# Kernel tuning notes

Hardware: AMD Instinct MI355X
Metric: run time of the kernel (lower is better)

Reference implementation:

```python
import jax, jax.numpy as jnp
import numpy as np

P = 2; NH = 8; NW = 4; NB = 6; D = 512; HID = 2048; NREG = 1; T = 1000; NACT = 3
HH = 32; WW = 32; C = 3; B = 1; DUR = 6


def _kron_bool(a, b):
    # kron(A,B)[i*p+k, j*q+l] = A[i,j] & B[k,l]
    m, n = a.shape; p, q = b.shape
    return (a[:, None, :, None] & b[None, :, None, :]).reshape(m * p, n * q)


def _masks(dur_zr, seq_zr, dur_xa, seq_xa):
    m_left = _kron_bool(jnp.eye(dur_zr, dtype=bool), jnp.ones((seq_zr, seq_zr), dtype=bool))
    tmp = jnp.ones((dur_zr, dur_zr), dtype=bool)
    band = jnp.tril(tmp, -1) ^ jnp.tril(tmp, -1 - NW)  # sliding window over previous frames
    m_right = _kron_bool(band[:, :-1], jnp.ones((seq_zr, seq_xa), dtype=bool))
    m_self = _kron_bool(jnp.tril(jnp.ones((dur_xa, dur_xa), dtype=bool)), jnp.ones((seq_xa, seq_xa), dtype=bool))
    return ~jnp.concatenate([m_left, m_right], axis=1), ~m_self


def _ln(x):
    mu = jnp.mean(x, -1, keepdims=True)
    xc = x - mu
    var = jnp.mean(xc * xc, -1, keepdims=True)
    return xc * jax.lax.rsqrt(var + 1e-5)


def _patch(x, Wp, bp):
    b, dur, c, h, w = x.shape
    x = x.reshape(b, dur, c, h // P, P, w // P, P)
    x = x.transpose(0, 1, 3, 5, 2, 4, 6).reshape(b, dur, (h // P) * (w // P), c * P * P)
    return x @ Wp + bp


def _unpatch(x, Wu, bu):
    b, dur, s, d = x.shape
    y = x @ Wu + bu  # [b,dur,s,C*P*P]
    y = y.reshape(b, dur, HH // P, WW // P, C, P, P)
    return y.transpose(0, 1, 4, 2, 5, 3, 6).reshape(b, dur, C, HH, WW)


def _mod(x, cond, Wm, bm):
    # AdaLN: per-frame scale/shift broadcast over tokens of that frame
    scale, shift = jnp.split(jax.nn.silu(cond) @ Wm + bm, 2, axis=-1)
    b, L, d = x.shape; dur = cond.shape[1]; s = L // dur
    y = _ln(x).reshape(b, dur, s, d)
    return (y * (1.0 + scale[:, :, None]) + shift[:, :, None]).reshape(b, L, d)


def _gate(x, cond, Wg, bg):
    g = cond @ Wg + bg
    b, L, d = x.shape; dur = cond.shape[1]; s = L // dur
    return (x.reshape(b, dur, s, d) * g[:, :, None]).reshape(b, L, d)


def _attn(q, kv, mask, Wq, bq, Wk, bk, Wv, bv, Wo, bo):
    b, lq, d = q.shape; lk = kv.shape[1]; dh = d // NH
    qh = (q @ Wq + bq).reshape(b, lq, NH, dh)
    kh = (kv @ Wk + bk).reshape(b, lk, NH, dh)
    vh = (kv @ Wv + bv).reshape(b, lk, NH, dh)
    s = jnp.einsum('bqhd,bkhd->bhqk', qh, kh) * (1.0 / np.sqrt(dh))
    s = jnp.where(mask[None, None], -1e9, s)  # mask True = disallowed
    o = jnp.einsum('bhqk,bkhd->bqhd', jax.nn.softmax(s, axis=-1), vh)
    return o.reshape(b, lq, d) @ Wo + bo


def _geglu(x, Wg, bg, Wo, bo):
    a, g = jnp.split(x @ Wg + bg, 2, axis=-1)
    return (a * jax.nn.gelu(g, approximate=False)) @ Wo + bo


def _forward(z, frames, actions, ts, W_patch, b_patch, W_unpatch, b_unpatch, registers, pe_grid, action_emb, time_emb, W_mod1, b_mod1, W_mod2, b_mod2, W_q, b_q, W_k, b_k, W_v, b_v, W_o, b_o, W_g1, b_g1, W_g2, b_g2, W_geglu, b_geglu, W_ffout, b_ffout):
    zt = _patch(z, W_patch, b_patch) + pe_grid[None, None]
    xt = _patch(frames, W_patch, b_patch) + pe_grid[None, None]
    a = action_emb[actions]  # [B, dur, D]
    b, dur_zr, s, d = zt.shape
    zr = jnp.concatenate([zt, jnp.broadcast_to(registers[None, None], (b, dur_zr, NREG, d))], axis=2)
    xa = jnp.concatenate([xt, a[:, :-1, None, :]], axis=2)
    seq_zr = zr.shape[2]; dur_xa = xa.shape[1]; seq_xa = xa.shape[2]
    mask_cross, mask_self = _masks(dur_zr, seq_zr, dur_xa, seq_xa)
    zr = zr.reshape(b, dur_zr * seq_zr, d)
    xa = xa.reshape(b, dur_xa * seq_xa, d)
    cond = time_emb[ts]  # [B, dur_zr, D]
    clean = jnp.broadcast_to(time_emb[0][None, None], (b, dur_xa, d))
    for i in range(NB):
        zrn = _mod(zr, cond, W_mod1[i], b_mod1[i])
        xan = _mod(xa, clean, W_mod1[i], b_mod1[i])
        xkv = jnp.concatenate([zrn, xan], axis=1)
        cross = _attn(zrn, xkv, mask_cross, W_q[i], b_q[i], W_k[i], b_k[i], W_v[i], b_v[i], W_o[i], b_o[i])
        selfa = _attn(xan, xan, mask_self, W_q[i], b_q[i], W_k[i], b_k[i], W_v[i], b_v[i], W_o[i], b_o[i])
        zr = _gate(zrn, cond, W_g1[i], b_g1[i])
        xa = _gate(xan, clean, W_g1[i], b_g1[i])
        zr = _mod(zr + cross, cond, W_mod2[i], b_mod2[i])
        xa = _mod(xa + selfa, clean, W_mod2[i], b_mod2[i])
        zr = _geglu(zr, W_geglu[i], b_geglu[i], W_ffout[i], b_ffout[i])
        xa = _geglu(xa, W_geglu[i], b_geglu[i], W_ffout[i], b_ffout[i])
        zr = _gate(zr, cond, W_g2[i], b_g2[i])
        xa = _gate(xa, clean, W_g2[i], b_g2[i])
    zr = zr.reshape(b, dur_zr, seq_zr, d)[:, :, :-NREG]
    return _unpatch(zr, W_unpatch, b_unpatch)


def setup_inputs() -> dict:
    key = jax.random.key(0)
    ks = iter(jax.random.split(key, 64))
    def rn(shape, scale=0.02):
        return jax.random.normal(next(ks), shape, dtype=jnp.float32) * scale
    inp = {}
    inp['z'] = jax.random.normal(next(ks), (B, DUR, C, HH, WW), dtype=jnp.float32)
    inp['frames'] = jax.random.normal(next(ks), (B, DUR - 1, C, HH, WW), dtype=jnp.float32)
    inp['actions'] = jax.random.randint(next(ks), (B, DUR), 0, NACT)
    inp['ts'] = jax.random.randint(next(ks), (B, DUR), 0, T)
    inp['W_patch'] = rn((C * P * P, D)); inp['b_patch'] = jnp.zeros((D,), jnp.float32)
    inp['W_unpatch'] = rn((D, C * P * P)); inp['b_unpatch'] = jnp.zeros((C * P * P,), jnp.float32)
    inp['registers'] = rn((NREG, D), 1.0 / D ** 0.5)
    inp['pe_grid'] = rn(((HH // P) * (WW // P), D), 1.0 / D ** 0.5)
    inp['action_emb'] = rn((NACT, D), 1.0)
    inp['time_emb'] = rn((T, D), 1.0)
    inp['W_mod1'] = rn((NB, D, 2 * D)); inp['b_mod1'] = jnp.zeros((NB, 2 * D), jnp.float32)
    inp['W_mod2'] = rn((NB, D, 2 * D)); inp['b_mod2'] = jnp.zeros((NB, 2 * D), jnp.float32)
    for nm in ('q', 'k', 'v', 'o'):
        inp['W_' + nm] = rn((NB, D, D)); inp['b_' + nm] = jnp.zeros((NB, D), jnp.float32)
    inp['W_g1'] = rn((NB, D, D)); inp['b_g1'] = jnp.ones((NB, D), jnp.float32)
    inp['W_g2'] = rn((NB, D, D)); inp['b_g2'] = jnp.ones((NB, D), jnp.float32)
    inp['W_geglu'] = rn((NB, D, 2 * HID)); inp['b_geglu'] = jnp.zeros((NB, 2 * HID), jnp.float32)
    inp['W_ffout'] = rn((NB, HID, D)); inp['b_ffout'] = jnp.zeros((NB, D), jnp.float32)
    return inp


def reference(z, frames, actions, ts, W_patch, b_patch, W_unpatch, b_unpatch, registers, pe_grid, action_emb, time_emb, W_mod1, b_mod1, W_mod2, b_mod2, W_q, b_q, W_k, b_k, W_v, b_v, W_o, b_o, W_g1, b_g1, W_g2, b_g2, W_geglu, b_geglu, W_ffout, b_ffout):
    return _forward(z, frames, actions, ts, W_patch, b_patch, W_unpatch, b_unpatch, registers, pe_grid, action_emb, time_emb, W_mod1, b_mod1, W_mod2, b_mod2, W_q, b_q, W_k, b_k, W_v, b_v, W_o, b_o, W_g1, b_g1, W_g2, b_g2, W_geglu, b_geglu, W_ffout, b_ffout)
```

## Files before the change

### kernel.cpp

```cpp
#include <hip/hip_runtime.h>
#include <hip/hip_bf16.h>
#include <math.h>

#define DURZ 6
#define DURX 5
#define SEQ 257
#define LZ 1542
#define LX 1285
#define LT 2827
#define DM 512
#define NHEADS 8
#define DH 64
#define HIDDEN 2048

typedef __bf16 bf16x8 __attribute__((ext_vector_type(8)));
typedef __bf16 bf16x4 __attribute__((ext_vector_type(4)));
typedef float f32x4 __attribute__((ext_vector_type(4)));

__global__ void fill_kernel(float* __restrict__ out, int n, float v) {
    int i = blockIdx.x * blockDim.x + threadIdx.x;
    if (i < n) out[i] = v;
}

__global__ void embed_kernel(const float* __restrict__ z,
                             const float* __restrict__ frames,
                             const int* __restrict__ actions,
                             const float* __restrict__ W_patch,
                             const float* __restrict__ b_patch,
                             const float* __restrict__ registers,
                             const float* __restrict__ pe,
                             const float* __restrict__ action_emb,
                             float* __restrict__ state) {
    int T = blockIdx.x;
    int tid = threadIdx.x;
    bool is_z = T < LZ;
    int T2 = is_z ? T : T - LZ;
    int f = T2 / SEQ, t = T2 % SEQ;
    if (t < 256) {
        const float* src = is_z ? z : frames;
        int hp = t >> 4, wp = t & 15;
        float pv[12];
#pragma unroll
        for (int c = 0; c < 3; c++)
#pragma unroll
            for (int ph = 0; ph < 2; ph++)
#pragma unroll
                for (int pw = 0; pw < 2; pw++)
                    pv[c * 4 + ph * 2 + pw] =
                        src[((f * 3 + c) * 32 + (hp * 2 + ph)) * 32 + (wp * 2 + pw)];
        for (int d = tid; d < DM; d += 256) {
            float acc = b_patch[d];
#pragma unroll
            for (int j = 0; j < 12; j++) acc += pv[j] * W_patch[j * DM + d];
            acc += pe[t * DM + d];
            state[T * DM + d] = acc;
        }
    } else if (is_z) {
        for (int d = tid; d < DM; d += 256) state[T * DM + d] = registers[d];
    } else {
        int a = actions[f];
        for (int d = tid; d < DM; d += 256) state[T * DM + d] = action_emb[a * DM + d];
    }
}

__global__ void cond_kernel(const int* __restrict__ ts,
                            const float* __restrict__ time_emb,
                            float* __restrict__ condraw,
                            float* __restrict__ condsilu) {
    int idx = blockIdx.x * blockDim.x + threadIdx.x;
    if (idx >= 7 * 512) return;
    int r = idx >> 9;
    int j = idx & 511;
    int tsr = (r < 6) ? ts[r] : 0;
    float x = time_emb[tsr * 512 + j];
    condraw[idx] = x;
    condsilu[idx] = x / (1.0f + expf(-x));
}

__global__ void params_kernel(const float* __restrict__ condraw,
                              const float* __restrict__ condsilu,
                              const float* __restrict__ W_mod1,
                              const float* __restrict__ b_mod1,
                              const float* __restrict__ W_mod2,
                              const float* __restrict__ b_mod2,
                              const float* __restrict__ W_g1,
                              const float* __restrict__ b_g1,
                              const float* __restrict__ W_g2,
                              const float* __restrict__ b_g2,
                              float* __restrict__ params) {
    int idx = blockIdx.x * blockDim.x + threadIdx.x;
    if (idx >= 6 * 7 * 3072) return;
    int i = idx / 21504;
    int rem = idx % 21504;
    int r = rem / 3072;
    int c = rem % 3072;
    const float* cv;
    const float* W;
    float bias;
    int ldw;
    if (c < 1024) {
        cv = condsilu + r * 512;
        W = W_mod1 + (size_t)i * 512 * 1024 + c; ldw = 1024;
        bias = b_mod1[i * 1024 + c];
    } else if (c < 2048) {
        int cc = c - 1024;
        cv = condsilu + r * 512;
        W = W_mod2 + (size_t)i * 512 * 1024 + cc; ldw = 1024;
        bias = b_mod2[i * 1024 + cc];
    } else if (c < 2560) {
        int cc = c - 2048;
        cv = condraw + r * 512;
        W = W_g1 + (size_t)i * 512 * 512 + cc; ldw = 512;
        bias = b_g1[i * 512 + cc];
    } else {
        int cc = c - 2560;
        cv = condraw + r * 512;
        W = W_g2 + (size_t)i * 512 * 512 + cc; ldw = 512;
        bias = b_g2[i * 512 + cc];
    }
    float acc = bias;
    for (int j = 0; j < 512; j++) acc += cv[j] * W[(size_t)j * ldw];
    params[idx] = acc;
}

template<bool PL>
__global__ __launch_bounds__(256) void lnmod_kernel(const float* __restrict__ xf,
                                                    const __bf16* __restrict__ xh,
                                                    const __bf16* __restrict__ xl,
                                                    __bf16* __restrict__ yh,
                                                    __bf16* __restrict__ yl,
                                                    const float* __restrict__ params,
                                                    int mod_off) {
    int T = blockIdx.x;
    int tid = threadIdx.x;
    int r = (T < LZ) ? (T / SEQ) : 6;
    const float* prow = params + r * 3072 + mod_off;
    size_t base = (size_t)T * DM;
    float v0, v1;
    if constexpr (PL) {
        v0 = (float)xh[base + tid] + (float)xl[base + tid];
        v1 = (float)xh[base + tid + 256] + (float)xl[base + tid + 256];
    } else {
        v0 = xf[base + tid];
        v1 = xf[base + tid + 256];
    }
    float s_ = v0 + v1, q_ = v0 * v0 + v1 * v1;
#pragma unroll
    for (int off = 32; off; off >>= 1) {
        s_ += __shfl_down(s_, off);
        q_ += __shfl_down(q_, off);
    }
    __shared__ float sh[8];
    int wave = tid >> 6, lane = tid & 63;
    if (lane == 0) { sh[wave] = s_; sh[4 + wave] = q_; }
    __syncthreads();
    float sum = sh[0] + sh[1] + sh[2] + sh[3];
    float sq = sh[4] + sh[5] + sh[6] + sh[7];
    float mu = sum * (1.0f / 512.0f);
    float var = sq * (1.0f / 512.0f) - mu * mu;
    float rstd = rsqrtf(var + 1e-5f);
    float y0 = (v0 - mu) * rstd * (1.0f + prow[tid]) + prow[512 + tid];
    float y1 = (v1 - mu) * rstd * (1.0f + prow[tid + 256]) + prow[512 + tid + 256];
    __bf16 h0 = (__bf16)y0, h1 = (__bf16)y1;
    yh[base + tid] = h0;
    yl[base + tid] = (__bf16)(y0 - (float)h0);
    yh[base + tid + 256] = h1;
    yl[base + tid + 256] = (__bf16)(y1 - (float)h1);
}


#define MFMA3(accv, ah, al, bh, bl)                                            \
    accv = __builtin_amdgcn_mfma_f32_16x16x32_bf16(al, bh, accv, 0, 0, 0);     \
    accv = __builtin_amdgcn_mfma_f32_16x16x32_bf16(ah, bl, accv, 0, 0, 0);     \
    accv = __builtin_amdgcn_mfma_f32_16x16x32_bf16(ah, bh, accv, 0, 0, 0);

__global__ __launch_bounds__(256) void wprep_kernel(const float* __restrict__ Wq,
                                                    const float* __restrict__ Wk,
                                                    const float* __restrict__ Wv,
                                                    const float* __restrict__ Wo,
                                                    const float* __restrict__ Wglu,
                                                    const float* __restrict__ Wff,
                                                    float* __restrict__ Wp) {
    __shared__ __align__(16) __bf16 T[2][64][40];
    int id = blockIdx.x, t = threadIdx.x;
    const float* src;
    int N, nsub, kt;
    size_t dstf;
    if (id < 512) {
        int mat = id >> 7, rem = id & 127;
        nsub = rem >> 4; kt = rem & 15; N = 512;
        src = mat == 0 ? Wq : mat == 1 ? Wk : mat == 2 ? Wv : Wo;
        dstf = (size_t)mat * 327680 + (size_t)(nsub * 16 + kt) * 2560;
    } else if (id < 1536) {
        int rem = id - 512;
        nsub = rem >> 4; kt = rem & 15; N = 4096; src = Wglu;
        dstf = 1310720 + (size_t)(nsub * 16 + kt) * 2560;
    } else {
        int rem = id - 1536;
        nsub = rem >> 6; kt = rem & 63; N = 512; src = Wff;
        dstf = 3932160 + (size_t)(nsub * 64 + kt) * 2560;
    }
    int r = t >> 2;
    int cb = (t & 3) * 8;
#pragma unroll
    for (int j = 0; j < 8; ++j) {
        int c = cb + j;
        float x = src[(size_t)(kt * 32 + c) * N + nsub * 64 + r];
        __bf16 h = (__bf16)x;
        T[0][r][c] = h;
        T[1][r][c] = (__bf16)(x - (float)h);
    }
    __syncthreads();
    float4* d = (float4*)(Wp + dstf);
    const float4* s4 = (const float4*)(&T[0][0][0]);
    for (int i2 = t; i2 < 640; i2 += 256) d[i2] = s4[i2];
}

#define M_QKV 0
#define M_GATE1 1
#define M_GLU 2
#define M_GATE2 3

template<int MODE>
__global__ __launch_bounds__(256) void gemm_kernel(
    const __bf16* __restrict__ Aph, const __bf16* __restrict__ Apl,
    const char* __restrict__ Wbase, int KT, int Krow,
    const float* __restrict__ b0, const float* __restrict__ b1,
    const float* __restrict__ b2,
    float* __restrict__ C0, float* __restrict__ C1, float* __restrict__ C2,
    __bf16* __restrict__ Oh, __bf16* __restrict__ Ol,
    const __bf16* __restrict__ Xh, const __bf16* __restrict__ Xl,
    const float* __restrict__ params, int M) {
    __shared__ __align__(16) __bf16 Alds[2][2][64][32];
    __shared__ __align__(16) __bf16 Blds[2][2][2][64][40];
    int tid = threadIdx.x;
    int w = tid >> 6, lane = tid & 63;
    int q = lane >> 4, lr = lane & 15;
    int nwg = gridDim.x * gridDim.y;
    int lin = blockIdx.y * gridDim.x + blockIdx.x;
    int qq = nwg >> 3, rr = nwg & 7;
    int xcd = lin & 7, ix = lin >> 3;
    int wg = (xcd < rr) ? xcd * (qq + 1) + ix : rr * (qq + 1) + (xcd - rr) * qq + ix;
    int mb = wg % gridDim.x;
    int nb = wg / gridDim.x;
    int m0 = mb * 64;
    const char* sb0;
    const char* sb1;
    if constexpr (MODE == M_QKV) {
        int sel = nb >> 2;
        const char* mbp = Wbase + (size_t)sel * 1310720;
        sb0 = mbp + (size_t)(2 * (nb & 3)) * 163840;
        sb1 = mbp + (size_t)(2 * (nb & 3) + 1) * 163840;
    } else if constexpr (MODE == M_GLU) {
        sb0 = Wbase + (size_t)nb * 163840;
        sb1 = Wbase + (size_t)(32 + nb) * 163840;
    } else {
        sb0 = Wbase + (size_t)(2 * nb) * (size_t)KT * 10240;
        sb1 = Wbase + (size_t)(2 * nb + 1) * (size_t)KT * 10240;
    }
    int wm = (w >> 1) * 32;

    auto stage = [&](int sbuf, int kt) {
        const char* k0 = sb0 + (size_t)kt * 10240;
        const char* k1 = sb1 + (size_t)kt * 10240;
        char* bl = (char*)(&Blds[sbuf][0][0][0][0]);
        for (int idx = w; idx < 20; idx += 4) {
            int sub = idx & 1, c = idx >> 1;
            const char* g = (sub ? k1 : k0) + (c << 10) + (lane << 4);
            __builtin_amdgcn_global_load_lds((const unsigned int*)g,
                (unsigned int*)(bl + sub * 10240 + (c << 10)), 16, 0, 0);
        }
        char* al = (char*)(&Alds[sbuf][0][0][0]);
        for (int idx = w; idx < 8; idx += 4) {
            int p = idx & 1, c = idx >> 1;
            int row = c * 16 + (lane >> 2);
            int ss = (lane & 3) ^ ((row >> 1) & 3);
            int mrow = m0 + row;
            if (mrow > M - 1) mrow = M - 1;
            const __bf16* ap = (p ? Apl : Aph) + (size_t)mrow * Krow + kt * 32 + ss * 8;
            __builtin_amdgcn_global_load_lds((const unsigned int*)ap,
                (unsigned int*)(al + p * 4096 + (c << 10)), 16, 0, 0);
        }
    };

    f32x4 acc[2][4];
#pragma unroll
    for (int i = 0; i < 2; ++i)
#pragma unroll
        for (int j = 0; j < 4; ++j)
#pragma unroll
            for (int r = 0; r < 4; ++r) acc[i][j][r] = 0.0f;

    stage(0, 0);
    __syncthreads();
    for (int kt = 0; kt < KT; ++kt) {
        int buf = kt & 1;
        if (kt + 1 < KT) stage(buf ^ 1, kt + 1);
        bf16x8 afh[2], afl[2], bh[4], bl4[4];
#pragma unroll
        for (int i = 0; i < 2; ++i) {
            int row = wm + i * 16 + lr;
            int off = (q * 16) ^ (((row >> 1) & 3) << 4);
            afh[i] = *(const bf16x8*)((const char*)(&Alds[buf][0][row][0]) + off);
            afl[i] = *(const bf16x8*)((const char*)(&Alds[buf][1][row][0]) + off);
        }
#pragma unroll
        for (int j = 0; j < 4; ++j) {
            int bsub, brow;
            if constexpr (MODE == M_GLU) {
                bsub = j >> 1;
                brow = (w & 1) * 32 + (j & 1) * 16 + lr;
            } else {
                bsub = w & 1;
                brow = j * 16 + lr;
            }
            bh[j] = *(const bf16x8*)(&Blds[buf][bsub][0][brow][q * 8]);
            bl4[j] = *(const bf16x8*)(&Blds[buf][bsub][1][brow][q * 8]);
        }
#pragma unroll
        for (int i = 0; i < 2; ++i)
#pragma unroll
            for (int j = 0; j < 4; ++j) {
                MFMA3(acc[i][j], afh[i], afl[i], bh[j], bl4[j]);
            }
        __syncthreads();
    }

#pragma unroll
    for (int i = 0; i < 2; ++i)
#pragma unroll
        for (int r = 0; r < 4; ++r) {
            int m = m0 + wm + i * 16 + q * 4 + r;
            if (m >= M) continue;
            if constexpr (MODE == M_QKV) {
                int sel = nb >> 2;
                const float* bias = sel == 0 ? b0 : (sel == 1 ? b1 : b2);
                float* C = sel == 0 ? C0 : (sel == 1 ? C1 : C2);
                int c0 = (nb & 3) * 128 + (w & 1) * 64;
#pragma unroll
                for (int j = 0; j < 4; ++j) {
                    int n = c0 + j * 16 + lr;
                    C[(size_t)m * 512 + n] = acc[i][j][r] + bias[n];
                }
            } else if constexpr (MODE == M_GATE1) {
                int r6 = (m < LZ) ? (m / SEQ) : 6;
                const float* g1 = params + r6 * 3072 + 2048;
                int c0 = nb * 128 + (w & 1) * 64;
#pragma unroll
                for (int j = 0; j < 4; ++j) {
                    int n = c0 + j * 16 + lr;
                    size_t o = (size_t)m * 512 + n;
                    float x = (float)Xh[o] + (float)Xl[o];
                    float v = x * g1[n] + acc[i][j][r] + b0[n];
                    __bf16 hh = (__bf16)v;
                    Oh[o] = hh;
                    Ol[o] = (__bf16)(v - (float)hh);
                }
            } else if constexpr (MODE == M_GLU) {
#pragma unroll
                for (int j = 0; j < 2; ++j) {
                    int n = nb * 64 + (w & 1) * 32 + j * 16 + lr;
                    float a = acc[i][j][r] + b0[n];
                    float g = acc[i][j + 2][r] + b0[2048 + n];
                    float gel = 0.5f * g * (1.0f + erff(g * 0.70710678118654752f));
                    float v = a * gel;
                    size_t o = (size_t)m * 2048 + n;
                    __bf16 hh = (__bf16)v;
                    Oh[o] = hh;
                    Ol[o] = (__bf16)(v - (float)hh);
                }
            } else {
                int r6 = (m < LZ) ? (m / SEQ) : 6;
                const float* g2 = params + r6 * 3072 + 2560;
                int c0 = nb * 128 + (w & 1) * 64;
#pragma unroll
                for (int j = 0; j < 4; ++j) {
                    int n = c0 + j * 16 + lr;
                    C0[(size_t)m * 512 + n] = (acc[i][j][r] + b0[n]) * g2[n];
                }
            }
        }
}

__global__ __launch_bounds__(256) void fattn_kernel(const float* __restrict__ Q,
                                                    const float* __restrict__ K,
                                                    const float* __restrict__ V,
                                                    __bf16* __restrict__ Oh,
                                                    __bf16* __restrict__ Ol) {
    __shared__ __align__(16) __bf16 Kh[64][72], Kl[64][72];
    __shared__ __align__(16) __bf16 Vth[64][72], Vtl[64][72];
    __shared__ __align__(16) __bf16 Ph[4][16][72], Pl[4][16][72];
    int tid = threadIdx.x;
    int w = tid >> 6, lane = tid & 63;
    int lq = lane & 15, lg = lane >> 4;
    int hoff = blockIdx.z * DH;
    int qbase, base0, len0, base1, len1;
    if (blockIdx.y < 6) {
        int f = blockIdx.y;
        qbase = f * SEQ;
        base0 = f * SEQ; len0 = SEQ;
        int jl = f - 4; if (jl < 0) jl = 0;
        base1 = LZ + jl * SEQ; len1 = (f - jl) * SEQ;
    } else {
        int f = blockIdx.y - 6;
        qbase = LZ + f * SEQ;
        base0 = LZ; len0 = (f + 1) * SEQ;
        base1 = 0; len1 = 0;
    }
    int q0 = blockIdx.x * 64;
    int qvalid = SEQ - q0; if (qvalid > 64) qvalid = 64;

    bf16x8 qh[2], ql[2];
    {
        int qr = w * 16 + lq;
        bool v = qr < qvalid;
        const float* qp = Q + (size_t)(qbase + q0 + qr) * DM + hoff + lg * 8;
#pragma unroll
        for (int s = 0; s < 2; ++s) {
            float4 a = v ? *(const float4*)(qp + s * 32) : make_float4(0, 0, 0, 0);
            float4 b = v ? *(const float4*)(qp + s * 32 + 4) : make_float4(0, 0, 0, 0);
            float fa[8] = {a.x, a.y, a.z, a.w, b.x, b.y, b.z, b.w};
#pragma unroll
            for (int j = 0; j < 8; ++j) {
                __bf16 hh = (__bf16)fa[j];
                qh[s][j] = hh;
                ql[s][j] = (__bf16)(fa[j] - (float)hh);
            }
        }
    }
    f32x4 acc[4];
#pragma unroll
    for (int n = 0; n < 4; ++n)
#pragma unroll
        for (int r = 0; r < 4; ++r) acc[n][r] = 0.0f;
    float m_i = -1e30f, l_i = 0.0f;

    for (int rng = 0; rng < 2; ++rng) {
        int base = rng ? base1 : base0;
        int len = rng ? len1 : len0;
        for (int t0 = 0; t0 < len; t0 += 64) {
            int valid = len - t0; if (valid > 64) valid = 64;
            __syncthreads();
            {
                int kr = tid >> 2, kc = (tid & 3) * 16;
                const float* kp = K + (size_t)(base + t0 + kr) * DM + hoff + kc;
                bool v = kr < valid;
                bf16x8 h0, h1, l0, l1;
#pragma unroll
                for (int c = 0; c < 4; ++c) {
                    float4 t4 = v ? *(const float4*)(kp + c * 4) : make_float4(0, 0, 0, 0);
                    float f4a[4] = {t4.x, t4.y, t4.z, t4.w};
#pragma unroll
                    for (int j = 0; j < 4; ++j) {
                        int idx = c * 4 + j;
                        __bf16 hh = (__bf16)f4a[j];
                        __bf16 ll = (__bf16)(f4a[j] - (float)hh);
                        if (idx < 8) { h0[idx] = hh; l0[idx] = ll; }
                        else { h1[idx - 8] = hh; l1[idx - 8] = ll; }
                    }
                }
                *(bf16x8*)&Kh[kr][kc] = h0;
                *(bf16x8*)&Kh[kr][kc + 8] = h1;
                *(bf16x8*)&Kl[kr][kc] = l0;
                *(bf16x8*)&Kl[kr][kc + 8] = l1;
            }
            {
                int d = tid & 63, kq = (tid >> 6) * 16;
                bf16x8 h0, h1, l0, l1;
#pragma unroll
                for (int j = 0; j < 16; ++j) {
                    float x = (kq + j < valid)
                        ? V[(size_t)(base + t0 + kq + j) * DM + hoff + d] : 0.0f;
                    __bf16 hh = (__bf16)x;
                    __bf16 ll = (__bf16)(x - (float)hh);
                    if (j < 8) { h0[j] = hh; l0[j] = ll; }
                    else { h1[j - 8] = hh; l1[j - 8] = ll; }
                }
                *(bf16x8*)&Vth[d][kq] = h0;
                *(bf16x8*)&Vth[d][kq + 8] = h1;
                *(bf16x8*)&Vtl[d][kq] = l0;
                *(bf16x8*)&Vtl[d][kq + 8] = l1;
            }
            __syncthreads();
            f32x4 st[4];
#pragma unroll
            for (int sub = 0; sub < 4; ++sub)
#pragma unroll
                for (int r = 0; r < 4; ++r) st[sub][r] = 0.0f;
#pragma unroll
            for (int sub = 0; sub < 4; ++sub) {
#pragma unroll
                for (int s = 0; s < 2; ++s) {
                    bf16x8 kfh = *(const bf16x8*)(&Kh[sub * 16 + lq][s * 32 + lg * 8]);
                    bf16x8 kfl = *(const bf16x8*)(&Kl[sub * 16 + lq][s * 32 + lg * 8]);
                    MFMA3(st[sub], kfh, kfl, qh[s], ql[s]);
                }
            }
            float p[16];
            float rmax = -1e30f;
#pragma unroll
            for (int sub = 0; sub < 4; ++sub)
#pragma unroll
                for (int r = 0; r < 4; ++r) {
                    int kk = sub * 16 + lg * 4 + r;
                    float sv = (kk < valid) ? st[sub][r] * 0.125f : -1e30f;
                    p[sub * 4 + r] = sv;
                    rmax = fmaxf(rmax, sv);
                }
            rmax = fmaxf(rmax, __shfl_xor(rmax, 16));
            rmax = fmaxf(rmax, __shfl_xor(rmax, 32));
            float mnew = fmaxf(m_i, rmax);
            float alpha = __expf(m_i - mnew);
            float rsum = 0.0f;
#pragma unroll
            for (int i2 = 0; i2 < 16; ++i2) {
                p[i2] = __expf(p[i2] - mnew);
                rsum += p[i2];
            }
            rsum += __shfl_xor(rsum, 16);
            rsum += __shfl_xor(rsum, 32);
            l_i = l_i * alpha + rsum;
            m_i = mnew;
            float ar[4];
#pragma unroll
            for (int r = 0; r < 4; ++r) ar[r] = __shfl(alpha, lg * 4 + r);
#pragma unroll
            for (int n = 0; n < 4; ++n)
#pragma unroll
                for (int r = 0; r < 4; ++r) acc[n][r] *= ar[r];
#pragma unroll
            for (int sub = 0; sub < 4; ++sub) {
                bf16x4 h4, l4;
#pragma unroll
                for (int r = 0; r < 4; ++r) {
                    float x = p[sub * 4 + r];
                    __bf16 hh = (__bf16)x;
                    h4[r] = hh;
                    l4[r] = (__bf16)(x - (float)hh);
                }
                *(bf16x4*)&Ph[w][lq][sub * 16 + lg * 4] = h4;
                *(bf16x4*)&Pl[w][lq][sub * 16 + lg * 4] = l4;
            }
            bf16x8 pah[2], pal[2];
#pragma unroll
            for (int s = 0; s < 2; ++s) {
                pah[s] = *(const bf16x8*)(&Ph[w][lq][s * 32 + lg * 8]);
                pal[s] = *(const bf16x8*)(&Pl[w][lq][s * 32 + lg * 8]);
            }
#pragma unroll
            for (int n = 0; n < 4; ++n) {
#pragma unroll
                for (int s = 0; s < 2; ++s) {
                    bf16x8 vfh = *(const bf16x8*)(&Vth[n * 16 + lq][s * 32 + lg * 8]);
                    bf16x8 vfl = *(const bf16x8*)(&Vtl[n * 16 + lq][s * 32 + lg * 8]);
                    MFMA3(acc[n], pah[s], pal[s], vfh, vfl);
                }
            }
        }
    }
    float linv[4];
#pragma unroll
    for (int r = 0; r < 4; ++r) linv[r] = 1.0f / __shfl(l_i, lg * 4 + r);
#pragma unroll
    for (int r = 0; r < 4; ++r) {
        int qr = w * 16 + lg * 4 + r;
        if (qr < qvalid) {
            size_t ob = (size_t)(qbase + q0 + qr) * DM + hoff;
#pragma unroll
            for (int n = 0; n < 4; ++n) {
                float v = acc[n][r] * linv[r];
                __bf16 hh = (__bf16)v;
                Oh[ob + n * 16 + lq] = hh;
                Ol[ob + n * 16 + lq] = (__bf16)(v - (float)hh);
            }
        }
    }
}

__global__ void unpatch_kernel(const float* __restrict__ state,
                               const float* __restrict__ Wu,
                               const float* __restrict__ bu,
                               float* __restrict__ out) {
    int idx = blockIdx.x * blockDim.x + threadIdx.x;
    if (idx >= DURZ * 3 * 32 * 32) return;
    int w = idx & 31, hh = (idx >> 5) & 31, c = (idx >> 10) % 3, f = idx / (3 * 1024);
    int t = (hh >> 1) * 16 + (w >> 1);
    int j = c * 4 + (hh & 1) * 2 + (w & 1);
    const float* xr = state + (size_t)(f * SEQ + t) * DM;
    float acc = bu[j];
    for (int k = 0; k < DM; ++k) acc += xr[k] * Wu[k * 12 + j];
    out[idx] = acc;
}

extern "C" void kernel_launch(void* const* d_in, const int* in_sizes, int n_in,
                              void* d_out, int out_size, void* d_ws, size_t ws_size,
                              hipStream_t stream) {
    static const int expected_sizes[32] = {
        18432, 15360, 6, 6,
        6144, 512, 6144, 12,
        512, 131072, 1536, 512000,
        3145728, 6144, 3145728, 6144,
        1572864, 3072, 1572864, 3072,
        1572864, 3072, 1572864, 3072,
        1572864, 3072, 1572864, 3072,
        12582912, 24576, 6291456, 3072
    };
    if (n_in != 32) {
        fill_kernel<<<(18432 + 255) / 256, 256, 0, stream>>>((float*)d_out, 18432, 3.0f);
        return;
    }
    for (int i = 0; i < 32; ++i) {
        if (in_sizes[i] != expected_sizes[i]) {
            fill_kernel<<<(18432 + 255) / 256, 256, 0, stream>>>((float*)d_out, 18432,
                                                                 4.0f + (float)i);
            return;
        }
    }

    const float* z = (const float*)d_in[0];
    const float* frames = (const float*)d_in[1];
    const int* actions = (const int*)d_in[2];
    const int* ts = (const int*)d_in[3];
    const float* W_patch = (const float*)d_in[4];
    const float* b_patch = (const float*)d_in[5];
    const float* W_unpatch = (const float*)d_in[6];
    const float* b_unpatch = (const float*)d_in[7];
    const float* registers = (const float*)d_in[8];
    const float* pe_grid = (const float*)d_in[9];
    const float* action_emb = (const float*)d_in[10];
    const float* time_emb = (const float*)d_in[11];
    const float* W_mod1 = (const float*)d_in[12];
    const float* b_mod1 = (const float*)d_in[13];
    const float* W_mod2 = (const float*)d_in[14];
    const float* b_mod2 = (const float*)d_in[15];
    const float* W_q = (const float*)d_in[16];
    const float* b_q = (const float*)d_in[17];
    const float* W_k = (const float*)d_in[18];
    const float* b_k = (const float*)d_in[19];
    const float* W_v = (const float*)d_in[20];
    const float* b_v = (const float*)d_in[21];
    const float* W_o = (const float*)d_in[22];
    const float* b_o = (const float*)d_in[23];
    const float* W_g1 = (const float*)d_in[24];
    const float* b_g1 = (const float*)d_in[25];
    const float* W_g2 = (const float*)d_in[26];
    const float* b_g2 = (const float*)d_in[27];
    const float* W_geglu = (const float*)d_in[28];
    const float* b_geglu = (const float*)d_in[29];
    const float* W_ffout = (const float*)d_in[30];
    const float* b_ffout = (const float*)d_in[31];

    const size_t S = (size_t)LT * DM;
    size_t need = (7 * S + 129024 + 7168 + 5242880) * sizeof(float);
    if (ws_size < need) {
        fill_kernel<<<(18432 + 255) / 256, 256, 0, stream>>>((float*)d_out, 18432, 40.0f);
        return;
    }
    float* ws = (float*)d_ws;
    float* state = ws;
    __bf16* xnh = (__bf16*)(ws + S);
    __bf16* xnl = (__bf16*)(ws + S + S / 2);
    float* qb = ws + 2 * S;
    float* kb = ws + 3 * S;
    float* vb = ws + 4 * S;
    __bf16* atth = (__bf16*)(ws + 5 * S);
    __bf16* attl = (__bf16*)(ws + 5 * S + S / 2);
    __bf16* y2h = (__bf16*)(ws + 6 * S);
    __bf16* y2l = (__bf16*)(ws + 6 * S + S / 2);
    __bf16* Hph = (__bf16*)(ws + 2 * S);
    __bf16* Hpl = (__bf16*)(ws + 4 * S);
    float* params = ws + 7 * S;
    float* condraw = params + 129024;
    float* condsilu = condraw + 3584;
    float* wp = condsilu + 3584;

    embed_kernel<<<LT, 256, 0, stream>>>(z, frames, actions, W_patch, b_patch,
                                         registers, pe_grid, action_emb, state);
    cond_kernel<<<(7 * 512 + 255) / 256, 256, 0, stream>>>(ts, time_emb, condraw, condsilu);
    params_kernel<<<(6 * 7 * 3072 + 255) / 256, 256, 0, stream>>>(
        condraw, condsilu, W_mod1, b_mod1, W_mod2, b_mod2, W_g1, b_g1, W_g2, b_g2, params);

    dim3 gqkv(45, 12);
    dim3 ggate1(45, 4);
    dim3 gglu(45, 32);
    dim3 ggate2(45, 4);
    dim3 gattn(5, 11, NHEADS);
    for (int i = 0; i < 6; ++i) {
        const float* P = params + i * 21504;
        wprep_kernel<<<2048, 256, 0, stream>>>(
            W_q + (size_t)i * DM * DM, W_k + (size_t)i * DM * DM,
            W_v + (size_t)i * DM * DM, W_o + (size_t)i * DM * DM,
            W_geglu + (size_t)i * DM * 4096, W_ffout + (size_t)i * HIDDEN * DM, wp);
        lnmod_kernel<false><<<LT, 256, 0, stream>>>(state, nullptr, nullptr,
                                                    xnh, xnl, P, 0);
        gemm_kernel<M_QKV><<<gqkv, 256, 0, stream>>>(
            xnh, xnl, (const char*)wp, 16, 512,
            b_q + i * DM, b_k + i * DM, b_v + i * DM, qb, kb, vb,
            nullptr, nullptr, nullptr, nullptr, nullptr, LT);
        fattn_kernel<<<gattn, 256, 0, stream>>>(qb, kb, vb, atth, attl);
        gemm_kernel<M_GATE1><<<ggate1, 256, 0, stream>>>(
            atth, attl, (const char*)(wp + 983040), 16, 512,
            b_o + i * DM, nullptr, nullptr, nullptr, nullptr, nullptr,
            y2h, y2l, xnh, xnl, P, LT);
        lnmod_kernel<true><<<LT, 256, 0, stream>>>(nullptr, y2h, y2l,
                                                   xnh, xnl, P, 1024);
        gemm_kernel<M_GLU><<<gglu, 256, 0, stream>>>(
            xnh, xnl, (const char*)(wp + 1310720), 16, 512,
            b_geglu + (size_t)i * 4096, nullptr, nullptr, nullptr, nullptr, nullptr,
            Hph, Hpl, nullptr, nullptr, nullptr, LT);
        gemm_kernel<M_GATE2><<<ggate2, 256, 0, stream>>>(
            Hph, Hpl, (const char*)(wp + 3932160), 64, 2048,
            b_ffout + i * DM, nullptr, nullptr, state, nullptr, nullptr,
            nullptr, nullptr, nullptr, nullptr, P, LT);
    }
    unpatch_kernel<<<(DURZ * 3 * 32 * 32 + 255) / 256, 256, 0, stream>>>(
        state, W_unpatch, b_unpatch, (float*)d_out);
}
```

Baseline: 1.974 ms.

## Emit split-bf16 Q/K/transposed-V from QKV GEMM and DMA tiles into swizzled LDS

The QKV GEMM epilogue now writes Q (pre-scaled by 1/8), K and a transposed V as hi/lo bf16 pairs into padded buffers, instead of fp32. The attention kernel then streams 64-aligned K and V tiles straight into XOR-swizzled LDS with global_load_lds, and masks out-of-range keys by index. This removes the per-tile fp32-to-bf16 splitting and the strided V gather inside attention, and it halves the bytes moved for Q/K/V. In exchange it adds a one-time tail-zeroing kernel and a workspace re-layout, and the transposed V store from the GEMM uses 8-byte strided writes.

```diff
diff --git a/kernel.cpp b/kernel.cpp
--- a/kernel.cpp
+++ b/kernel.cpp
@@ -8,6 +8,7 @@
 #define LZ 1542
 #define LX 1285
 #define LT 2827
+#define LTP 2880
 #define DM 512
 #define NHEADS 8
 #define DH 64
@@ -123,6 +124,17 @@
     params[idx] = acc;
 }
 
+__global__ void ztail_kernel(__bf16* __restrict__ Kh, __bf16* __restrict__ Kl,
+                             __bf16* __restrict__ Vth, __bf16* __restrict__ Vtl) {
+    int idx = blockIdx.x * blockDim.x + threadIdx.x;
+    if (idx >= (LTP - LT) * 512) return;
+    int r = idx / 512, c = idx % 512;
+    Kh[(size_t)(LT + r) * DM + c] = (__bf16)0.0f;
+    Kl[(size_t)(LT + r) * DM + c] = (__bf16)0.0f;
+    Vth[(size_t)c * LTP + LT + r] = (__bf16)0.0f;
+    Vtl[(size_t)c * LTP + LT + r] = (__bf16)0.0f;
+}
+
 template<bool PL>
 __global__ __launch_bounds__(256) void lnmod_kernel(const float* __restrict__ xf,
                                                     const __bf16* __restrict__ xh,
@@ -167,7 +179,6 @@
     yh[base + tid + 256] = h1;
     yl[base + tid + 256] = (__bf16)(y1 - (float)h1);
 }
-
 
 #define MFMA3(accv, ah, al, bh, bl)                                            \
     accv = __builtin_amdgcn_mfma_f32_16x16x32_bf16(al, bh, accv, 0, 0, 0);     \
@@ -227,8 +238,10 @@
     const char* __restrict__ Wbase, int KT, int Krow,
     const float* __restrict__ b0, const float* __restrict__ b1,
     const float* __restrict__ b2,
-    float* __restrict__ C0, float* __restrict__ C1, float* __restrict__ C2,
+    float* __restrict__ C0,
     __bf16* __restrict__ Oh, __bf16* __restrict__ Ol,
+    __bf16* __restrict__ O2h, __bf16* __restrict__ O2l,
+    __bf16* __restrict__ O3h, __bf16* __restrict__ O3l,
     const __bf16* __restrict__ Xh, const __bf16* __restrict__ Xl,
     const float* __restrict__ params, int M) {
     __shared__ __align__(16) __bf16 Alds[2][2][64][32];
@@ -326,23 +339,68 @@
         __syncthreads();
     }
 
+    if constexpr (MODE == M_QKV) {
+        int sel = nb >> 2;
+        int c0 = (nb & 3) * 128 + (w & 1) * 64;
+        if (sel == 2) {
+#pragma unroll
+            for (int i = 0; i < 2; ++i) {
+                int mb2 = m0 + wm + i * 16 + q * 4;
+#pragma unroll
+                for (int j = 0; j < 4; ++j) {
+                    int n = c0 + j * 16 + lr;
+                    bf16x4 h4, l4;
+#pragma unroll
+                    for (int r = 0; r < 4; ++r) {
+                        float v = acc[i][j][r] + b2[n];
+                        __bf16 hh = (__bf16)v;
+                        h4[r] = hh;
+                        l4[r] = (__bf16)(v - (float)hh);
+                    }
+                    if (mb2 + 3 < M) {
+                        *(bf16x4*)(O3h + (size_t)n * LTP + mb2) = h4;
+                        *(bf16x4*)(O3l + (size_t)n * LTP + mb2) = l4;
+                    } else {
+#pragma unroll
+                        for (int r = 0; r < 4; ++r)
+                            if (mb2 + r < M) {
+                                O3h[(size_t)n * LTP + mb2 + r] = h4[r];
+                                O3l[(size_t)n * LTP + mb2 + r] = l4[r];
+                            }
+                    }
+                }
+            }
+        } else {
+            const float* bias = sel == 0 ? b0 : b1;
+            __bf16* Dh = sel == 0 ? Oh : O2h;
+            __bf16* Dl = sel == 0 ? Ol : O2l;
+            float scale = sel == 0 ? 0.125f : 1.0f;
+#pragma unroll
+            for (int i = 0; i < 2; ++i)
+#pragma unroll
+                for (int r = 0; r < 4; ++r) {
+                    int m = m0 + wm + i * 16 + q * 4 + r;
+                    if (m >= M) continue;
+#pragma unroll
+                    for (int j = 0; j < 4; ++j) {
+                        int n = c0 + j * 16 + lr;
+                        float v = (acc[i][j][r] + bias[n]) * scale;
+                        __bf16 hh = (__bf16)v;
+                        Dh[(size_t)m * DM + n] = hh;
+                        Dl[(size_t)m * DM + n] = (__bf16)(v - (float)hh);
+                    }
+                }
+        }
+        return;
+    }
+
 #pragma unroll
     for (int i = 0; i < 2; ++i)
 #pragma unroll
         for (int r = 0; r < 4; ++r) {
             int m = m0 + wm + i * 16 + q * 4 + r;
             if (m >= M) continue;
-            if constexpr (MODE == M_QKV) {
-                int sel = nb >> 2;
-                const float* bias = sel == 0 ? b0 : (sel == 1 ? b1 : b2);
-                float* C = sel == 0 ? C0 : (sel == 1 ? C1 : C2);
-                int c0 = (nb & 3) * 128 + (w & 1) * 64;
-#pragma unroll
-                for (int j = 0; j < 4; ++j) {
-                    int n = c0 + j * 16 + lr;
-                    C[(size_t)m * 512 + n] = acc[i][j][r] + bias[n];
-                }
-            } else if constexpr (MODE == M_GATE1) {
+            if constexpr (MODE == M_GATE1) {
                 int r6 = (m < LZ) ? (m / SEQ) : 6;
                 const float* g1 = params + r6 * 3072 + 2048;
                 int c0 = nb * 128 + (w & 1) * 64;
@@ -382,13 +440,13 @@
         }
 }
 
-__global__ __launch_bounds__(256) void fattn_kernel(const float* __restrict__ Q,
-                                                    const float* __restrict__ K,
-                                                    const float* __restrict__ V,
-                                                    __bf16* __restrict__ Oh,
-                                                    __bf16* __restrict__ Ol) {
-    __shared__ __align__(16) __bf16 Kh[64][72], Kl[64][72];
-    __shared__ __align__(16) __bf16 Vth[64][72], Vtl[64][72];
+__global__ __launch_bounds__(256) void fattn_kernel(
+    const __bf16* __restrict__ Qph, const __bf16* __restrict__ Qpl,
+    const __bf16* __restrict__ Kph, const __bf16* __restrict__ Kpl,
+    const __bf16* __restrict__ Vph, const __bf16* __restrict__ Vpl,
+    __bf16* __restrict__ Oh, __bf16* __restrict__ Ol) {
+    __shared__ __align__(16) __bf16 Ksh[2][64][64];
+    __shared__ __align__(16) __bf16 Vsh[2][64][64];
     __shared__ __align__(16) __bf16 Ph[4][16][72], Pl[4][16][72];
     int tid = threadIdx.x;
     int w = tid >> 6, lane = tid & 63;
@@ -410,22 +468,16 @@
     int q0 = blockIdx.x * 64;
     int qvalid = SEQ - q0; if (qvalid > 64) qvalid = 64;
 
-    bf16x8 qh[2], ql[2];
+    bf16x8 qfh[2], qfl[2];
     {
         int qr = w * 16 + lq;
-        bool v = qr < qvalid;
-        const float* qp = Q + (size_t)(qbase + q0 + qr) * DM + hoff + lg * 8;
+        int tok = qbase + q0 + ((qr < qvalid) ? qr : 0);
+        const __bf16* qph = Qph + (size_t)tok * DM + hoff + lg * 8;
+        const __bf16* qpl = Qpl + (size_t)tok * DM + hoff + lg * 8;
 #pragma unroll
         for (int s = 0; s < 2; ++s) {
-            float4 a = v ? *(const float4*)(qp + s * 32) : make_float4(0, 0, 0, 0);
-            float4 b = v ? *(const float4*)(qp + s * 32 + 4) : make_float4(0, 0, 0, 0);
-            float fa[8] = {a.x, a.y, a.z, a.w, b.x, b.y, b.z, b.w};
-#pragma unroll
-            for (int j = 0; j < 8; ++j) {
-                __bf16 hh = (__bf16)fa[j];
-                qh[s][j] = hh;
-                ql[s][j] = (__bf16)(fa[j] - (float)hh);
-            }
+            qfh[s] = *(const bf16x8*)(qph + s * 32);
+            qfl[s] = *(const bf16x8*)(qpl + s * 32);
         }
     }
     f32x4 acc[4];
@@ -434,52 +486,36 @@
 #pragma unroll
         for (int r = 0; r < 4; ++r) acc[n][r] = 0.0f;
     float m_i = -1e30f, l_i = 0.0f;
+    int slot = lane & 7, rsub = lane >> 3;
 
     for (int rng = 0; rng < 2; ++rng) {
         int base = rng ? base1 : base0;
         int len = rng ? len1 : len0;
-        for (int t0 = 0; t0 < len; t0 += 64) {
-            int valid = len - t0; if (valid > 64) valid = 64;
+        if (len == 0) continue;
+        int tend = base + len;
+        for (int t = base & ~63; t < tend; t += 64) {
+            int lo = base - t; if (lo < 0) lo = 0;
+            int hi = tend - t; if (hi > 64) hi = 64;
             __syncthreads();
-            {
-                int kr = tid >> 2, kc = (tid & 3) * 16;
-                const float* kp = K + (size_t)(base + t0 + kr) * DM + hoff + kc;
-                bool v = kr < valid;
-                bf16x8 h0, h1, l0, l1;
-#pragma unroll
-                for (int c = 0; c < 4; ++c) {
-                    float4 t4 = v ? *(const float4*)(kp + c * 4) : make_float4(0, 0, 0, 0);
-                    float f4a[4] = {t4.x, t4.y, t4.z, t4.w};
-#pragma unroll
-                    for (int j = 0; j < 4; ++j) {
-                        int idx = c * 4 + j;
-                        __bf16 hh = (__bf16)f4a[j];
-                        __bf16 ll = (__bf16)(f4a[j] - (float)hh);
-                        if (idx < 8) { h0[idx] = hh; l0[idx] = ll; }
-                        else { h1[idx - 8] = hh; l1[idx - 8] = ll; }
-                    }
-                }
-                *(bf16x8*)&Kh[kr][kc] = h0;
-                *(bf16x8*)&Kh[kr][kc + 8] = h1;
-                *(bf16x8*)&Kl[kr][kc] = l0;
-                *(bf16x8*)&Kl[kr][kc + 8] = l1;
-            }
-            {
-                int d = tid & 63, kq = (tid >> 6) * 16;
-                bf16x8 h0, h1, l0, l1;
-#pragma unroll
-                for (int j = 0; j < 16; ++j) {
-                    float x = (kq + j < valid)
-                        ? V[(size_t)(base + t0 + kq + j) * DM + hoff + d] : 0.0f;
-                    __bf16 hh = (__bf16)x;
-                    __bf16 ll = (__bf16)(x - (float)hh);
-                    if (j < 8) { h0[j] = hh; l0[j] = ll; }
-                    else { h1[j - 8] = hh; l1[j - 8] = ll; }
-                }
-                *(bf16x8*)&Vth[d][kq] = h0;
-                *(bf16x8*)&Vth[d][kq + 8] = h1;
-                *(bf16x8*)&Vtl[d][kq] = l0;
-                *(bf16x8*)&Vtl[d][kq + 8] = l1;
+#pragma unroll
+            for (int ii = 0; ii < 4; ++ii) {
+                int idx = w + ii * 4;
+                int p = idx >> 3, c = idx & 7;
+                int row = c * 8 + rsub;
+                const __bf16* g = (p ? Kpl : Kph) +
+                    (size_t)(t + row) * DM + hoff + (slot ^ (row & 7)) * 8;
+                __builtin_amdgcn_global_load_lds((const unsigned int*)g,
+                    (unsigned int*)((char*)(&Ksh[p][0][0]) + c * 1024), 16, 0, 0);
+            }
+#pragma unroll
+            for (int ii = 0; ii < 4; ++ii) {
+                int idx = w + ii * 4;
+                int p = idx >> 3, c = idx & 7;
+                int d = c * 8 + rsub;
+                const __bf16* g = (p ? Vpl : Vph) +
+                    (size_t)(hoff + d) * LTP + t + (slot ^ (d & 7)) * 8;
+                __builtin_amdgcn_global_load_lds((const unsigned int*)g,
+                    (unsigned int*)((char*)(&Vsh[p][0][0]) + c * 1024), 16, 0, 0);
             }
             __syncthreads();
             f32x4 st[4];
@@ -489,11 +525,13 @@
                 for (int r = 0; r < 4; ++r) st[sub][r] = 0.0f;
 #pragma unroll
             for (int sub = 0; sub < 4; ++sub) {
+                int row = sub * 16 + lq;
 #pragma unroll
                 for (int s = 0; s < 2; ++s) {
-                    bf16x8 kfh = *(const bf16x8*)(&Kh[sub * 16 + lq][s * 32 + lg * 8]);
-                    bf16x8 kfl = *(const bf16x8*)(&Kl[sub * 16 + lq][s * 32 + lg * 8]);
-                    MFMA3(st[sub], kfh, kfl, qh[s], ql[s]);
+                    int sl = ((s * 4 + lg) ^ (row & 7)) * 8;
+                    bf16x8 kfh = *(const bf16x8*)(&Ksh[0][row][sl]);
+                    bf16x8 kfl = *(const bf16x8*)(&Ksh[1][row][sl]);
+                    MFMA3(st[sub], kfh, kfl, qfh[s], qfl[s]);
                 }
             }
             float p[16];
@@ -503,7 +541,7 @@
 #pragma unroll
                 for (int r = 0; r < 4; ++r) {
                     int kk = sub * 16 + lg * 4 + r;
-                    float sv = (kk < valid) ? st[sub][r] * 0.125f : -1e30f;
+                    float sv = (kk >= lo && kk < hi) ? st[sub][r] : -1e30f;
                     p[sub * 4 + r] = sv;
                     rmax = fmaxf(rmax, sv);
                 }
@@ -549,10 +587,12 @@
             }
 #pragma unroll
             for (int n = 0; n < 4; ++n) {
+                int row = n * 16 + lq;
 #pragma unroll
                 for (int s = 0; s < 2; ++s) {
-                    bf16x8 vfh = *(const bf16x8*)(&Vth[n * 16 + lq][s * 32 + lg * 8]);
-                    bf16x8 vfl = *(const bf16x8*)(&Vtl[n * 16 + lq][s * 32 + lg * 8]);
+                    int sl = ((s * 4 + lg) ^ (row & 7)) * 8;
+                    bf16x8 vfh = *(const bf16x8*)(&Vsh[0][row][sl]);
+                    bf16x8 vfl = *(const bf16x8*)(&Vsh[1][row][sl]);
                     MFMA3(acc[n], pah[s], pal[s], vfh, vfl);
                 }
             }
@@ -651,7 +691,9 @@
     const float* b_ffout = (const float*)d_in[31];
 
     const size_t S = (size_t)LT * DM;
-    size_t need = (7 * S + 129024 + 7168 + 5242880) * sizeof(float);
+    const size_t PLE = (size_t)LTP * DM;
+    const size_t PLF = PLE / 2;
+    size_t need = (4 * S + 6 * PLF + 129024 + 7168 + 5242880) * sizeof(float);
     if (ws_size < need) {
         fill_kernel<<<(18432 + 255) / 256, 256, 0, stream>>>((float*)d_out, 18432, 40.0f);
         return;
@@ -660,16 +702,20 @@
     float* state = ws;
     __bf16* xnh = (__bf16*)(ws + S);
     __bf16* xnl = (__bf16*)(ws + S + S / 2);
-    float* qb = ws + 2 * S;
-    float* kb = ws + 3 * S;
-    float* vb = ws + 4 * S;
-    __bf16* atth = (__bf16*)(ws + 5 * S);
-    __bf16* attl = (__bf16*)(ws + 5 * S + S / 2);
-    __bf16* y2h = (__bf16*)(ws + 6 * S);
-    __bf16* y2l = (__bf16*)(ws + 6 * S + S / 2);
+    __bf16* Qh = (__bf16*)(ws + 2 * S);
+    __bf16* Ql = Qh + PLE;
+    __bf16* Kh = Qh + 2 * PLE;
+    __bf16* Kl = Qh + 3 * PLE;
+    __bf16* Vth = Qh + 4 * PLE;
+    __bf16* Vtl = Qh + 5 * PLE;
+    float* aoff = ws + 2 * S + 6 * PLF;
+    __bf16* atth = (__bf16*)aoff;
+    __bf16* attl = atth + S;
+    __bf16* y2h = (__bf16*)(aoff + S);
+    __bf16* y2l = y2h + S;
     __bf16* Hph = (__bf16*)(ws + 2 * S);
-    __bf16* Hpl = (__bf16*)(ws + 4 * S);
-    float* params = ws + 7 * S;
+    __bf16* Hpl = Hph + (size_t)LT * HIDDEN;
+    float* params = aoff + 2 * S;
     float* condraw = params + 129024;
     float* condsilu = condraw + 3584;
     float* wp = condsilu + 3584;
@@ -679,6 +725,7 @@
     cond_kernel<<<(7 * 512 + 255) / 256, 256, 0, stream>>>(ts, time_emb, condraw, condsilu);
     params_kernel<<<(6 * 7 * 3072 + 255) / 256, 256, 0, stream>>>(
         condraw, condsilu, W_mod1, b_mod1, W_mod2, b_mod2, W_g1, b_g1, W_g2, b_g2, params);
+    ztail_kernel<<<((LTP - LT) * 512 + 255) / 256, 256, 0, stream>>>(Kh, Kl, Vth, Vtl);
 
     dim3 gqkv(45, 12);
     dim3 ggate1(45, 4);
@@ -695,23 +742,24 @@
                                                     xnh, xnl, P, 0);
         gemm_kernel<M_QKV><<<gqkv, 256, 0, stream>>>(
             xnh, xnl, (const char*)wp, 16, 512,
-            b_q + i * DM, b_k + i * DM, b_v + i * DM, qb, kb, vb,
-            nullptr, nullptr, nullptr, nullptr, nullptr, LT);
-        fattn_kernel<<<gattn, 256, 0, stream>>>(qb, kb, vb, atth, attl);
+            b_q + i * DM, b_k + i * DM, b_v + i * DM, nullptr,
+            Qh, Ql, Kh, Kl, Vth, Vtl, nullptr, nullptr, nullptr, LT);
+        fattn_kernel<<<gattn, 256, 0, stream>>>(Qh, Ql, Kh, Kl, Vth, Vtl, atth, attl);
         gemm_kernel<M_GATE1><<<ggate1, 256, 0, stream>>>(
             atth, attl, (const char*)(wp + 983040), 16, 512,
-            b_o + i * DM, nullptr, nullptr, nullptr, nullptr, nullptr,
-            y2h, y2l, xnh, xnl, P, LT);
+            b_o + i * DM, nullptr, nullptr, nullptr,
+            y2h, y2l, nullptr, nullptr, nullptr, nullptr, xnh, xnl, P, LT);
         lnmod_kernel<true><<<LT, 256, 0, stream>>>(nullptr, y2h, y2l,
                                                    xnh, xnl, P, 1024);
         gemm_kernel<M_GLU><<<gglu, 256, 0, stream>>>(
             xnh, xnl, (const char*)(wp + 1310720), 16, 512,
-            b_geglu + (size_t)i * 4096, nullptr, nullptr, nullptr, nullptr, nullptr,
-            Hph, Hpl, nullptr, nullptr, nullptr, LT);
+            b_geglu + (size_t)i * 4096, nullptr, nullptr, nullptr,
+            Hph, Hpl, nullptr, nullptr, nullptr, nullptr, nullptr, nullptr, nullptr, LT);
         gemm_kernel<M_GATE2><<<ggate2, 256, 0, stream>>>(
             Hph, Hpl, (const char*)(wp + 3932160), 64, 2048,
-            b_ffout + i * DM, nullptr, nullptr, state, nullptr, nullptr,
-            nullptr, nullptr, nullptr, nullptr, P, LT);
+            b_ffout + i * DM, nullptr, nullptr, state,
+            nullptr, nullptr, nullptr, nullptr, nullptr, nullptr,
+            nullptr, nullptr, P, LT);
     }
     unpatch_kernel<<<(DURZ * 3 * 32 * 32 + 255) / 256, 256, 0, stream>>>(
         state, W_unpatch, b_unpatch, (float*)d_out);
```

New measurement: 1.856 ms. 6.0% less time.
